# Optimization experiments

Hardware: AMD Instinct MI355X
Metric: run time of the kernel (lower is better)

## Reference

```python
import jax, jax.numpy as jnp
import numpy as np

D_MODEL = 1024
N_HEADS = 16
D_K = D_MODEL // N_HEADS  # 64
SCALE = 0.125             # attention_scale = 1/sqrt(d_k)
ROPE_BASE = 10000.0
NEG_INF = -1e30


def setup_inputs() -> dict:
    key = jax.random.key(0)
    k1, k2, k3 = jax.random.split(key, 3)
    B, S = 2, 2048
    x = jax.random.normal(k1, (B, S, D_MODEL), jnp.float32)
    # torch Linear(d_model, 3*d_model, bias=False): stored here as [in, out]
    w_qkv = jax.random.normal(k2, (D_MODEL, 3 * D_MODEL), jnp.float32) * (D_MODEL ** -0.5)
    w_o = jax.random.normal(k3, (D_MODEL, D_MODEL), jnp.float32) * (D_MODEL ** -0.5)
    return {"x": x, "w_qkv": w_qkv, "w_o": w_o}


def _rotary(x):
    # x: [B, H, S, D]; standard half-split rotary over sequence positions
    S, D = x.shape[2], x.shape[3]
    inv_freq = 1.0 / (ROPE_BASE ** (jnp.arange(0, D, 2, dtype=jnp.float32) / D))  # [D/2]
    freqs = jnp.arange(S, dtype=jnp.float32)[:, None] * inv_freq[None, :]          # [S, D/2]
    cos = jnp.cos(freqs)[None, None]  # [1,1,S,D/2]
    sin = jnp.sin(freqs)[None, None]
    x1, x2 = jnp.split(x, 2, axis=-1)
    return jnp.concatenate([x1 * cos + x2 * sin, -x1 * sin + x2 * cos], axis=-1).astype(x.dtype)


def reference(x, w_qkv, w_o):
    B, S, _ = x.shape
    qkv = x @ w_qkv                                        # [B,S,3*D_MODEL]
    qkv = qkv.reshape(B, S, 3, N_HEADS, D_K).transpose(2, 0, 3, 1, 4)  # [3,B,H,S,Dk]
    q, k, v = qkv[0], qkv[1], qkv[2]
    q = _rotary(q)
    k = _rotary(k)
    scores = jnp.einsum('bhqd,bhkd->bhqk', q, k) * SCALE   # [B,H,S,S]
    causal = jnp.tril(jnp.ones((S, S), dtype=bool))
    scores = jnp.where(causal, scores, NEG_INF)
    attn = jax.nn.softmax(scores, axis=-1)
    out = jnp.einsum('bhqk,bhkd->bhqd', attn, v)           # [B,H,S,Dk]
    out = out.transpose(0, 2, 1, 3).reshape(B, S, D_MODEL)
    return out @ w_o
```

## Files before the change

### kernel.cpp

```cpp
#include <hip/hip_runtime.h>

typedef short bf16x8 __attribute__((ext_vector_type(8)));
typedef short bf16x4 __attribute__((ext_vector_type(4)));
typedef float f32x4 __attribute__((ext_vector_type(4)));
typedef float f32x16 __attribute__((ext_vector_type(16)));
typedef int i32x4 __attribute__((ext_vector_type(4)));

#define DEVI static __device__ __forceinline__

DEVI unsigned short f2b(float f) {
  unsigned u = __float_as_uint(f);
  u += 0x7FFFu + ((u >> 16) & 1u);
  return (unsigned short)(u >> 16);
}

DEVI void gload16(const void* g, void* l) {
  __builtin_amdgcn_global_load_lds((const __attribute__((address_space(1))) void*)g,
                                   (__attribute__((address_space(3))) void*)l, 16, 0, 0);
}

DEVI void pl32swap(int a, int b, int& outa, int& outb) {
#if __has_builtin(__builtin_amdgcn_permlane32_swap)
  auto r = __builtin_amdgcn_permlane32_swap(a, b, false, false);
  outa = ((const int*)&r)[0];
  outb = ((const int*)&r)[1];
#else
  int bp = __shfl_xor(b, 32);
  int ap = __shfl_xor(a, 32);
  outa = (threadIdx.x & 32) ? bp : a;
  outb = (threadIdx.x & 32) ? b : ap;
#endif
}

DEVI float halfmax(float x) {
  int o0, o1;
  pl32swap(__float_as_int(x), __float_as_int(x), o0, o1);
  return fmaxf(__int_as_float(o0), __int_as_float(o1));
}
DEVI float halfsum(float x) {
  int o0, o1;
  pl32swap(__float_as_int(x), __float_as_int(x), o0, o1);
  return __int_as_float(o0) + __int_as_float(o1);
}

__global__ void rope_table_kernel(float2* __restrict__ cst) {
  int i = blockIdx.x * 256 + threadIdx.x;
  int s = i >> 5, j = i & 31;
  float inv = powf(10000.0f, -(float)j * (1.0f / 32.0f));
  float a = (float)s * inv;
  cst[i] = make_float2(cosf(a), sinf(a));
}

__global__ void cvt_x_kernel(const float* __restrict__ x, unsigned short* __restrict__ xb) {
  int i = blockIdx.x * 256 + threadIdx.x;
  float4 v = ((const float4*)x)[i];
  ushort4 o;
  o.x = f2b(v.x); o.y = f2b(v.y); o.z = f2b(v.z); o.w = f2b(v.w);
  ((ushort4*)xb)[i] = o;
}

__global__ void transpose2_kernel(const float* __restrict__ W1, unsigned short* __restrict__ WT1,
                                  const float* __restrict__ W2, unsigned short* __restrict__ WT2) {
  __shared__ float tile[32][33];
  int bx = blockIdx.x;
  const float* W; unsigned short* WT; int N;
  if (bx < 96) { W = W1; WT = WT1; N = 3072; }
  else         { W = W2; WT = WT2; N = 1024; bx -= 96; }
  const int K = 1024;
  int n0 = bx * 32, k0 = blockIdx.y * 32;
  int tx = threadIdx.x, ty = threadIdx.y;
#pragma unroll
  for (int i = 0; i < 32; i += 8)
    tile[ty + i][tx] = W[(size_t)(k0 + ty + i) * N + n0 + tx];
  __syncthreads();
#pragma unroll
  for (int i = 0; i < 32; i += 8)
    WT[(size_t)(n0 + ty + i) * K + k0 + tx] = f2b(tile[tx][ty + i]);
}

DEVI void gemm_mainloop(const unsigned short* __restrict__ A, const unsigned short* __restrict__ B,
                        unsigned short* As, unsigned short* Bs,
                        int m0, int n0, int lane, int wid, int wr, int wc,
                        f32x4 acc[4][4]) {
  const int srow = lane >> 3;
  const int scc = ((lane & 7) ^ srow) * 8;
  const int rx = lane & 7;
  auto stage = [&](int k0, int nb) {
    unsigned short* Ad = As + nb * 8192;
    unsigned short* Bd = Bs + nb * 8192;
#pragma unroll
    for (int i = 0; i < 4; ++i) {
      const int c = i * 4 + wid;
      const int row = c * 8 + srow;
      gload16(A + (size_t)(m0 + row) * 1024 + k0 + scc, (char*)Ad + c * 1024);
      gload16(B + (size_t)(n0 + row) * 1024 + k0 + scc, (char*)Bd + c * 1024);
    }
  };
  auto compute = [&](int nb) {
    const unsigned short* Ab = As + nb * 8192;
    const unsigned short* Bb = Bs + nb * 8192;
#pragma unroll
    for (int kk = 0; kk < 64; kk += 32) {
      const int cc = (((kk >> 3) + (lane >> 4)) ^ rx) * 8;
      bf16x8 a[4], b[4];
#pragma unroll
      for (int mi = 0; mi < 4; ++mi)
        a[mi] = *(const bf16x8*)&Ab[(wr * 64 + mi * 16 + (lane & 15)) * 64 + cc];
#pragma unroll
      for (int ni = 0; ni < 4; ++ni)
        b[ni] = *(const bf16x8*)&Bb[(wc * 64 + ni * 16 + (lane & 15)) * 64 + cc];
      __builtin_amdgcn_s_setprio(1);
#pragma unroll
      for (int mi = 0; mi < 4; ++mi)
#pragma unroll
        for (int ni = 0; ni < 4; ++ni)
          acc[mi][ni] = __builtin_amdgcn_mfma_f32_16x16x32_bf16(a[mi], b[ni], acc[mi][ni], 0, 0, 0);
      __builtin_amdgcn_s_setprio(0);
    }
  };
  stage(0, 0);
  stage(64, 1);
  for (int t = 0; t < 15; ++t) {
    asm volatile("s_waitcnt vmcnt(8)" ::: "memory");
    __builtin_amdgcn_s_barrier();
    compute(t & 1);
    __builtin_amdgcn_s_barrier();
    if (t < 14) stage((t + 2) * 64, t & 1);
  }
  asm volatile("s_waitcnt vmcnt(0)" ::: "memory");
  __builtin_amdgcn_s_barrier();
  compute(1);
}

__global__ __launch_bounds__(256, 2) void gemm_qkv_kernel(
    const unsigned short* __restrict__ Xb, const unsigned short* __restrict__ WT,
    const float2* __restrict__ cst,
    unsigned short* __restrict__ Qb, unsigned short* __restrict__ Kb,
    unsigned short* __restrict__ VTb) {
  __shared__ unsigned short As[2][8192];
  __shared__ unsigned short Bs[2][8192];
  const int lane = threadIdx.x & 63, wid = threadIdx.x >> 6;
  const int flat = blockIdx.y * 24 + blockIdx.x;
  const int nf = (flat & 7) * 96 + (flat >> 3);
  const int bx = nf % 24, by = nf / 24;
  const int m0 = by * 128, n0 = bx * 128;
  const int wr = wid >> 1, wc = wid & 1;
  f32x4 acc[4][4] = {};
  gemm_mainloop(Xb, WT, &As[0][0], &Bs[0][0], m0, n0, lane, wid, wr, wc, acc);

  __syncthreads();
  unsigned short* slab = (unsigned short*)((char*)&As[0][0] + wid * 9216);
  const int n_base = n0 + wc * 64;
  const int ty = n_base >> 10;
  const int h = (n_base & 1023) >> 6;
  const int qrow = (lane >> 4) << 2;
  const int l15 = lane & 15;
  const int rlane = lane >> 3, clane = lane & 7;
  const int rowg = m0 + wr * 64;
  const int s_half = rowg & 2047, bb = rowg >> 11;

  if (ty < 2) {
    unsigned short* dst = (ty == 0) ? Qb : Kb;
#pragma unroll
    for (int mi = 0; mi < 4; ++mi) {
      const int rl0 = mi * 16 + qrow;
#pragma unroll
      for (int r = 0; r < 4; ++r) {
#pragma unroll
        for (int ni = 0; ni < 2; ++ni) {
          const int j = ni * 16 + l15;
          const float2 cs = cst[(s_half + rl0 + r) * 32 + j];
          const float x1 = acc[mi][ni][r], x2 = acc[mi][ni + 2][r];
          slab[(rl0 + r) * 72 + j]      = f2b(x1 * cs.x + x2 * cs.y);
          slab[(rl0 + r) * 72 + j + 32] = f2b(-x1 * cs.y + x2 * cs.x);
        }
      }
    }
    unsigned short* dp = dst + ((size_t)(bb * 16 + h) * 2048 + s_half) * 64;
#pragma unroll
    for (int i = 0; i < 8; ++i) {
      const int row = i * 8 + rlane;
      const bf16x8 v = *(const bf16x8*)&slab[row * 72 + clane * 8];
      *(bf16x8*)&dp[row * 64 + clane * 8] = v;
    }
  } else {
#pragma unroll
    for (int mi = 0; mi < 4; ++mi) {
      const int rl0 = mi * 16 + qrow;
#pragma unroll
      for (int ni = 0; ni < 4; ++ni) {
        const int d = ni * 16 + l15;
#pragma unroll
        for (int r = 0; r < 4; ++r)
          slab[d * 72 + rl0 + r] = f2b(acc[mi][ni][r]);
      }
    }
    unsigned short* vp = VTb + (size_t)(bb * 16 + h) * 64 * 2048 + s_half;
#pragma unroll
    for (int i = 0; i < 8; ++i) {
      const int d = i * 8 + rlane;
      const bf16x8 v = *(const bf16x8*)&slab[d * 72 + clane * 8];
      *(bf16x8*)&vp[(size_t)d * 2048 + clane * 8] = v;
    }
  }
}

DEVI void stage128(const unsigned short* __restrict__ Kh, const unsigned short* __restrict__ Vh,
                   int kbase, unsigned char* buf, int tid) {
  const int r = tid >> 3, c = tid & 7, cc = c ^ (r & 7);
  const int dst = (tid & ~63) * 16;
#pragma unroll
  for (int q = 0; q < 2; ++q) {
    unsigned char* b = buf + q * 16384;
    gload16(Kh + (size_t)(kbase + q * 64 + r) * 64 + cc * 8, b + dst);
    gload16(Vh + (size_t)r * 2048 + kbase + q * 64 + cc * 8, b + 8192 + dst);
  }
}

DEVI void build_pa(const f32x16& s, bf16x8& pa0, bf16x8& pa1) {
  int cw[8];
#pragma unroll
  for (int i = 0; i < 8; ++i)
    asm("v_cvt_pk_bf16_f32 %0, %1, %2" : "=v"(cw[i]) : "v"(s[2 * i]), "v"(s[2 * i + 1]));
  int a0, a1, b0, b1, a2, a3, b2, b3;
  pl32swap(cw[0], cw[2], a0, b0);
  pl32swap(cw[1], cw[3], a1, b1);
  pl32swap(cw[4], cw[6], a2, b2);
  pl32swap(cw[5], cw[7], a3, b3);
  pa0 = __builtin_bit_cast(bf16x8, (i32x4){a0, a1, b0, b1});
  pa1 = __builtin_bit_cast(bf16x8, (i32x4){a2, a3, b2, b3});
}

DEVI void attn_pair(const unsigned char* __restrict__ bufK, const unsigned char* __restrict__ bufV,
                    const bf16x8 qf[4], int kglob, bool diag1, int qg, int ln, int hi,
                    float& m2, float& l_run, f32x16& acc0, f32x16& acc1) {
  const float C = 0.125f * 1.44269504f;
  const int rx = ln & 7;
  f32x16 s0 = {}, s1 = {};
  {
    bf16x8 k0[4], k1[4];
#pragma unroll
    for (int j = 0; j < 4; ++j) {
      const int cc = (2 * j + hi) ^ rx;
      k0[j] = *(const bf16x8*)(bufK + ln * 128 + cc * 16);
      k1[j] = *(const bf16x8*)(bufK + (32 + ln) * 128 + cc * 16);
    }
    __builtin_amdgcn_s_setprio(1);
#pragma unroll
    for (int j = 0; j < 4; ++j) {
      s0 = __builtin_amdgcn_mfma_f32_32x32x16_bf16(k0[j], qf[j], s0, 0, 0, 0);
      s1 = __builtin_amdgcn_mfma_f32_32x32x16_bf16(k1[j], qf[j], s1, 0, 0, 0);
    }
    __builtin_amdgcn_s_setprio(0);
  }
  bf16x8 va[2][2], vb[2][2];
#pragma unroll
  for (int st = 0; st < 2; ++st)
#pragma unroll
    for (int p = 0; p < 2; ++p) {
      const int cc = (4 * st + 2 * p + hi) ^ rx;
      va[st][p] = *(const bf16x8*)(bufV + ln * 128 + cc * 16);
      vb[st][p] = *(const bf16x8*)(bufV + (ln + 32) * 128 + cc * 16);
    }

  if (diag1) {
#pragma unroll
    for (int r = 0; r < 16; ++r) {
      const int kg = kglob + 32 + (r & 3) + ((r >> 2) << 3) + (hi << 2);
      if (kg > qg) s1[r] = -1e30f;
    }
  }
  float mraw = fmaxf(s0[0], s1[0]);
#pragma unroll
  for (int r = 1; r < 16; ++r) mraw = fmaxf(mraw, fmaxf(s0[r], s1[r]));
  const float mlc = mraw * C;
  if (__any(mlc > m2 + 11.5416f)) {
    const float mnew = fmaxf(m2, halfmax(mlc));
    const float sc = exp2f(m2 - mnew);
    l_run *= sc;
#pragma unroll
    for (int r = 0; r < 16; ++r) { acc0[r] *= sc; acc1[r] *= sc; }
    m2 = mnew;
  }
  float ps0 = 0.f, ps1 = 0.f;
#pragma unroll
  for (int r = 0; r < 16; ++r) { s0[r] = exp2f(fmaf(s0[r], C, -m2)); ps0 += s0[r]; }
#pragma unroll
  for (int r = 0; r < 16; ++r) { s1[r] = exp2f(fmaf(s1[r], C, -m2)); ps1 += s1[r]; }
  l_run += ps0 + ps1;

  bf16x8 pa[2][2];
  build_pa(s0, pa[0][0], pa[0][1]);
  build_pa(s1, pa[1][0], pa[1][1]);

  __builtin_amdgcn_s_setprio(1);
#pragma unroll
  for (int st = 0; st < 2; ++st) {
    acc0 = __builtin_amdgcn_mfma_f32_32x32x16_bf16(va[st][0], pa[st][0], acc0, 0, 0, 0);
    acc1 = __builtin_amdgcn_mfma_f32_32x32x16_bf16(vb[st][0], pa[st][0], acc1, 0, 0, 0);
    acc0 = __builtin_amdgcn_mfma_f32_32x32x16_bf16(va[st][1], pa[st][1], acc0, 0, 0, 0);
    acc1 = __builtin_amdgcn_mfma_f32_32x32x16_bf16(vb[st][1], pa[st][1], acc1, 0, 0, 0);
  }
  __builtin_amdgcn_s_setprio(0);
}

DEVI void attn_single(const unsigned char* __restrict__ bufK, const unsigned char* __restrict__ bufV,
                      const bf16x8 qf[4], int kglob, int qg, int ln, int hi,
                      float& m2, float& l_run, f32x16& acc0, f32x16& acc1) {
  const float C = 0.125f * 1.44269504f;
  const int rx = ln & 7;
  f32x16 s0 = {};
  {
    bf16x8 k0[4];
#pragma unroll
    for (int j = 0; j < 4; ++j) {
      const int cc = (2 * j + hi) ^ rx;
      k0[j] = *(const bf16x8*)(bufK + ln * 128 + cc * 16);
    }
    __builtin_amdgcn_s_setprio(1);
#pragma unroll
    for (int j = 0; j < 4; ++j)
      s0 = __builtin_amdgcn_mfma_f32_32x32x16_bf16(k0[j], qf[j], s0, 0, 0, 0);
    __builtin_amdgcn_s_setprio(0);
  }
  bf16x8 va[2], vb[2];
#pragma unroll
  for (int p = 0; p < 2; ++p) {
    const int cc = (2 * p + hi) ^ rx;
    va[p] = *(const bf16x8*)(bufV + ln * 128 + cc * 16);
    vb[p] = *(const bf16x8*)(bufV + (ln + 32) * 128 + cc * 16);
  }
#pragma unroll
  for (int r = 0; r < 16; ++r) {
    const int kg = kglob + (r & 3) + ((r >> 2) << 3) + (hi << 2);
    if (kg > qg) s0[r] = -1e30f;
  }
  float mraw = s0[0];
#pragma unroll
  for (int r = 1; r < 16; ++r) mraw = fmaxf(mraw, s0[r]);
  const float mlc = mraw * C;
  if (__any(mlc > m2 + 11.5416f)) {
    const float mnew = fmaxf(m2, halfmax(mlc));
    const float sc = exp2f(m2 - mnew);
    l_run *= sc;
#pragma unroll
    for (int r = 0; r < 16; ++r) { acc0[r] *= sc; acc1[r] *= sc; }
    m2 = mnew;
  }
  float ps = 0.f;
#pragma unroll
  for (int r = 0; r < 16; ++r) { s0[r] = exp2f(fmaf(s0[r], C, -m2)); ps += s0[r]; }
  l_run += ps;

  bf16x8 pa0, pa1;
  build_pa(s0, pa0, pa1);
  __builtin_amdgcn_s_setprio(1);
  acc0 = __builtin_amdgcn_mfma_f32_32x32x16_bf16(va[0], pa0, acc0, 0, 0, 0);
  acc1 = __builtin_amdgcn_mfma_f32_32x32x16_bf16(vb[0], pa0, acc1, 0, 0, 0);
  acc0 = __builtin_amdgcn_mfma_f32_32x32x16_bf16(va[1], pa1, acc0, 0, 0, 0);
  acc1 = __builtin_amdgcn_mfma_f32_32x32x16_bf16(vb[1], pa1, acc1, 0, 0, 0);
  __builtin_amdgcn_s_setprio(0);
}

DEVI void write_partial(float* M, int slot, const f32x16& a0, const f32x16& a1,
                        float m2, float l) {
#pragma unroll
  for (int r = 0; r < 16; ++r) { M[slot + r] = a0[r]; M[slot + 16 + r] = a1[r]; }
  M[slot + 32] = m2;
  M[slot + 33] = l;
}

DEVI void write_merged(unsigned short* __restrict__ Ob, const float* M, int slot,
                       const f32x16& acc0, const f32x16& acc1, float m2, float l_run,
                       int bh, int q0, int ln, int hi) {
  const float mp = M[slot + 32], lp = M[slot + 33];
  const float m = fmaxf(m2, mp);
  const float eo = exp2f(m2 - m), ep = exp2f(mp - m);
  const float il = 1.0f / (l_run * eo + lp * ep);
  const int b = bh >> 4, h = bh & 15;
  unsigned short* ob = Ob + ((size_t)(b * 2048 + q0 + ln)) * 1024 + h * 64;
#pragma unroll
  for (int g = 0; g < 4; ++g) {
    ushort4 o0, o1;
    o0.x = f2b((acc0[4 * g + 0] * eo + M[slot + 4 * g + 0] * ep) * il);
    o0.y = f2b((acc0[4 * g + 1] * eo + M[slot + 4 * g + 1] * ep) * il);
    o0.z = f2b((acc0[4 * g + 2] * eo + M[slot + 4 * g + 2] * ep) * il);
    o0.w = f2b((acc0[4 * g + 3] * eo + M[slot + 4 * g + 3] * ep) * il);
    o1.x = f2b((acc1[4 * g + 0] * eo + M[slot + 16 + 4 * g + 0] * ep) * il);
    o1.y = f2b((acc1[4 * g + 1] * eo + M[slot + 16 + 4 * g + 1] * ep) * il);
    o1.z = f2b((acc1[4 * g + 2] * eo + M[slot + 16 + 4 * g + 2] * ep) * il);
    o1.w = f2b((acc1[4 * g + 3] * eo + M[slot + 16 + 4 * g + 3] * ep) * il);
    *(ushort4*)&ob[8 * g + 4 * hi]      = o0;
    *(ushort4*)&ob[32 + 8 * g + 4 * hi] = o1;
  }
}

__global__ __launch_bounds__(512, 2) void attn_kernel(
    const unsigned short* __restrict__ Qb, const unsigned short* __restrict__ Kb,
    const unsigned short* __restrict__ VTb, unsigned short* __restrict__ Ob) {
  __shared__ unsigned char smem[2][2][16384];
  const int tid = threadIdx.x;
  const int lane = tid & 63, wid = tid >> 6;
  const int ln = lane & 31, hi = lane >> 5;
  const int s = wid & 3, half = wid >> 2;
  const int bh = blockIdx.x;
  const int p = blockIdx.y;
  const int jA = 15 - p, jB = p;
  const unsigned short* Qh = Qb + (size_t)bh * 2048 * 64;
  const unsigned short* Kh = Kb + (size_t)bh * 2048 * 64;
  const unsigned short* Vh = VTb + (size_t)bh * 64 * 2048;

  f32x16 aA0 = {}, aA1 = {}, aB0 = {}, aB1 = {};
  float mA = -1e30f, lA = 0.f, mB = -1e30f, lB = 0.f;
  int it = 0;

  auto load_q = [&](int q0, bf16x8 qf[4]) {
    const unsigned short* pq = Qh + (size_t)(q0 + ln) * 64 + hi * 8;
#pragma unroll
    for (int t = 0; t < 4; ++t) qf[t] = *(const bf16x8*)(pq + t * 16);
  };
  auto run_phase = [&](int j, const bf16x8 qf[4], f32x16& acc0, f32x16& acc1,
                       float& m2, float& l_run, int q0, int nextFirst) {
    const int qg = q0 + ln;
    const int top = q0 >> 5;
    for (int kb = 0; kb <= j; ++kb, ++it) {
      const int nxt = (kb < j) ? (kb + 1) * 128 : nextFirst;
      if (nxt >= 0) stage128(Kh, Vh, nxt, &smem[(it + 1) & 1][0][0], tid);
      const unsigned char* bufK = &smem[it & 1][half][0];
      const unsigned char* bufV = bufK + 8192;
      const int t64 = 2 * kb + half;
      const int nv = top - 2 * t64 + 1;
      if (nv >= 2)
        attn_pair(bufK, bufV, qf, t64 * 64, top == 2 * t64 + 1, qg, ln, hi,
                  m2, l_run, acc0, acc1);
      else if (nv == 1)
        attn_single(bufK, bufV, qf, t64 * 64, qg, ln, hi, m2, l_run, acc0, acc1);
      __syncthreads();
    }
  };

  bf16x8 qfA[4];
  load_q(jA * 128 + s * 32, qfA);
  stage128(Kh, Vh, 0, &smem[0][0][0], tid);
  __syncthreads();
  run_phase(jA, qfA, aA0, aA1, mA, lA, jA * 128 + s * 32, 0);
  bf16x8 qfB[4];
  load_q(jB * 128 + s * 32, qfB);
  run_phase(jB, qfB, aB0, aB1, mB, lB, jB * 128 + s * 32, -1);

  lA = halfsum(lA);
  lB = halfsum(lB);

  float* M = (float*)&smem[0][0][0];
  const int slot = (s * 64 + lane) * 34;
  if (half == 1) write_partial(M, slot, aA0, aA1, mA, lA);
  __syncthreads();
  if (half == 0) write_merged(Ob, M, slot, aA0, aA1, mA, lA, bh, jA * 128 + s * 32, ln, hi);
  __syncthreads();
  if (half == 0) write_partial(M, slot, aB0, aB1, mB, lB);
  __syncthreads();
  if (half == 1) write_merged(Ob, M, slot, aB0, aB1, mB, lB, bh, jB * 128 + s * 32, ln, hi);
}

__global__ __launch_bounds__(256) void gemm_out_kernel(
    const unsigned short* __restrict__ Ob, const unsigned short* __restrict__ WoT,
    float* __restrict__ out) {
  __shared__ unsigned short As[2][8192];
  __shared__ unsigned short Bs[2][8192];
  const int lane = threadIdx.x & 63, wid = threadIdx.x >> 6;
  const int m0 = blockIdx.y * 128, n0 = blockIdx.x * 128;
  const int wr = wid >> 1, wc = wid & 1;
  f32x4 acc[4][4] = {};
  gemm_mainloop(Ob, WoT, &As[0][0], &Bs[0][0], m0, n0, lane, wid, wr, wc, acc);
#pragma unroll
  for (int mi = 0; mi < 4; ++mi) {
    const int mrow = m0 + wr * 64 + mi * 16 + ((lane >> 4) << 2);
#pragma unroll
    for (int ni = 0; ni < 4; ++ni) {
      const int n = n0 + wc * 64 + ni * 16 + (lane & 15);
#pragma unroll
      for (int r = 0; r < 4; ++r)
        out[(size_t)(mrow + r) * 1024 + n] = acc[mi][ni][r];
    }
  }
}

extern "C" void kernel_launch(void* const* d_in, const int* in_sizes, int n_in,
                              void* d_out, int out_size, void* d_ws, size_t ws_size,
                              hipStream_t stream) {
  const float* x     = (const float*)d_in[0];
  const float* w_qkv = (const float*)d_in[1];
  const float* w_o   = (const float*)d_in[2];
  float* out = (float*)d_out;
  char* ws = (char*)d_ws;

  const size_t MB = 1 << 20;
  float2* cst = (float2*)(ws);
  unsigned short* Xb  = (unsigned short*)(ws + (512 << 10));
  unsigned short* WqT = (unsigned short*)(ws + (512 << 10) + 8  * MB);
  unsigned short* WoT = (unsigned short*)(ws + (512 << 10) + 14 * MB);
  unsigned short* Qb  = (unsigned short*)(ws + (512 << 10) + 16 * MB);
  unsigned short* Kb  = (unsigned short*)(ws + (512 << 10) + 24 * MB);
  unsigned short* VTb = (unsigned short*)(ws + (512 << 10) + 32 * MB);
  unsigned short* Ob  = Xb;

  rope_table_kernel<<<dim3(256), dim3(256), 0, stream>>>(cst);
  cvt_x_kernel<<<dim3(4096), dim3(256), 0, stream>>>(x, Xb);
  transpose2_kernel<<<dim3(128, 32), dim3(32, 8), 0, stream>>>(w_qkv, WqT, w_o, WoT);
  gemm_qkv_kernel<<<dim3(24, 32), dim3(256), 0, stream>>>(Xb, WqT, cst, Qb, Kb, VTb);
  attn_kernel<<<dim3(32, 8), dim3(512), 0, stream>>>(Qb, Kb, VTb, Ob);
  gemm_out_kernel<<<dim3(8, 32), dim3(256), 0, stream>>>(Ob, WoT, out);
}
```

Measured before the change: 119.3 us.

## Flatten attention phases into one loop with two-deep K/V prefetch and vmcnt waits

Merges the two causal query-block phases into a single 17-iteration loop over K/V tiles. Each tile is staged two iterations ahead, and the code uses explicit s_waitcnt vmcnt plus raw s_barrier instead of __syncthreads. Both Q fragments are loaded up front. The goal is to hide global-to-LDS load latency behind compute and to avoid the full-drain barrier at every iteration, at the cost of higher register pressure from holding both Q sets. The vmcnt(4) count has to match the number of loads stage128 actually issues.

```diff
diff --git a/kernel.cpp b/kernel.cpp
--- a/kernel.cpp
+++ b/kernel.cpp
@@ -412,41 +412,48 @@
 
   f32x16 aA0 = {}, aA1 = {}, aB0 = {}, aB1 = {};
   float mA = -1e30f, lA = 0.f, mB = -1e30f, lB = 0.f;
-  int it = 0;
 
   auto load_q = [&](int q0, bf16x8 qf[4]) {
     const unsigned short* pq = Qh + (size_t)(q0 + ln) * 64 + hi * 8;
 #pragma unroll
     for (int t = 0; t < 4; ++t) qf[t] = *(const bf16x8*)(pq + t * 16);
   };
-  auto run_phase = [&](int j, const bf16x8 qf[4], f32x16& acc0, f32x16& acc1,
-                       float& m2, float& l_run, int q0, int nextFirst) {
-    const int qg = q0 + ln;
-    const int top = q0 >> 5;
-    for (int kb = 0; kb <= j; ++kb, ++it) {
-      const int nxt = (kb < j) ? (kb + 1) * 128 : nextFirst;
-      if (nxt >= 0) stage128(Kh, Vh, nxt, &smem[(it + 1) & 1][0][0], tid);
-      const unsigned char* bufK = &smem[it & 1][half][0];
-      const unsigned char* bufV = bufK + 8192;
-      const int t64 = 2 * kb + half;
-      const int nv = top - 2 * t64 + 1;
+  bf16x8 qfA[4], qfB[4];
+  const int q0A = jA * 128 + s * 32, q0B = jB * 128 + s * 32;
+  load_q(q0A, qfA);
+  load_q(q0B, qfB);
+  const int qgA = q0A + ln, qgB = q0B + ln;
+  const int topA = q0A >> 5, topB = q0B >> 5;
+
+  const int nT = 17;
+  auto kbase_of = [&](int i) { return (i <= jA) ? i * 128 : (i - jA - 1) * 128; };
+
+  stage128(Kh, Vh, kbase_of(0), &smem[0][0][0], tid);
+  stage128(Kh, Vh, kbase_of(1), &smem[1][0][0], tid);
+  for (int i = 0; i < nT; ++i) {
+    if (i < nT - 1) asm volatile("s_waitcnt vmcnt(4)" ::: "memory");
+    else            asm volatile("s_waitcnt vmcnt(0)" ::: "memory");
+    __builtin_amdgcn_s_barrier();
+    const unsigned char* bufK = &smem[i & 1][half][0];
+    const unsigned char* bufV = bufK + 8192;
+    if (i <= jA) {
+      const int t64 = 2 * i + half;
+      const int nv = topA - 2 * t64 + 1;
       if (nv >= 2)
-        attn_pair(bufK, bufV, qf, t64 * 64, top == 2 * t64 + 1, qg, ln, hi,
-                  m2, l_run, acc0, acc1);
+        attn_pair(bufK, bufV, qfA, t64 * 64, topA == 2 * t64 + 1, qgA, ln, hi, mA, lA, aA0, aA1);
       else if (nv == 1)
-        attn_single(bufK, bufV, qf, t64 * 64, qg, ln, hi, m2, l_run, acc0, acc1);
-      __syncthreads();
-    }
-  };
-
-  bf16x8 qfA[4];
-  load_q(jA * 128 + s * 32, qfA);
-  stage128(Kh, Vh, 0, &smem[0][0][0], tid);
-  __syncthreads();
-  run_phase(jA, qfA, aA0, aA1, mA, lA, jA * 128 + s * 32, 0);
-  bf16x8 qfB[4];
-  load_q(jB * 128 + s * 32, qfB);
-  run_phase(jB, qfB, aB0, aB1, mB, lB, jB * 128 + s * 32, -1);
+        attn_single(bufK, bufV, qfA, t64 * 64, qgA, ln, hi, mA, lA, aA0, aA1);
+    } else {
+      const int t64 = 2 * (i - jA - 1) + half;
+      const int nv = topB - 2 * t64 + 1;
+      if (nv >= 2)
+        attn_pair(bufK, bufV, qfB, t64 * 64, topB == 2 * t64 + 1, qgB, ln, hi, mB, lB, aB0, aB1);
+      else if (nv == 1)
+        attn_single(bufK, bufV, qfB, t64 * 64, qgB, ln, hi, mB, lB, aB0, aB1);
+    }
+    __builtin_amdgcn_s_barrier();
+    if (i + 2 < nT) stage128(Kh, Vh, kbase_of(i + 2), &smem[i & 1][0][0], tid);
+  }
 
   lA = halfsum(lA);
   lB = halfsum(lB);
@@ -455,11 +462,11 @@
   const int slot = (s * 64 + lane) * 34;
   if (half == 1) write_partial(M, slot, aA0, aA1, mA, lA);
   __syncthreads();
-  if (half == 0) write_merged(Ob, M, slot, aA0, aA1, mA, lA, bh, jA * 128 + s * 32, ln, hi);
+  if (half == 0) write_merged(Ob, M, slot, aA0, aA1, mA, lA, bh, q0A, ln, hi);
   __syncthreads();
   if (half == 0) write_partial(M, slot, aB0, aB1, mB, lB);
   __syncthreads();
-  if (half == 1) write_merged(Ob, M, slot, aB0, aB1, mB, lB, bh, jB * 128 + s * 32, ln, hi);
+  if (half == 1) write_merged(Ob, M, slot, aB0, aB1, mB, lB, bh, q0B, ln, hi);
 }
 
 __global__ __launch_bounds__(256) void gemm_out_kernel(
```

After: 124.6 us. 4.4% more time.
